# Kernel tuning notes

Hardware: AMD Instinct MI355X
Metric: run time of the kernel (lower is better)

## Reference

```python
import jax, jax.numpy as jnp
import numpy as np

EPS = 1.1920929e-07  # torch RMSNorm default eps = float32 finfo eps

def rms_norm(x, w):
    return x * jax.lax.rsqrt(jnp.mean(x * x, axis=-1, keepdims=True) + EPS) * w

def setup_inputs() -> dict:
    key = jax.random.key(0)
    ks = jax.random.split(key, 10)
    B, C, H, W = 8, 64, 48, 48
    E = C  # embed_dim = query_dim = key_dim = value_dim
    q = jax.random.normal(ks[0], (B, C, H, W), jnp.float32)
    k = jax.random.normal(ks[1], (B, C, H, W), jnp.float32)
    v = jax.random.normal(ks[2], (B, C, H, W), jnp.float32)
    s = 1.0 / np.sqrt(E)
    conv_w = jax.random.normal(ks[3], (C, C, 3, 3), jnp.float32) * (1.0 / np.sqrt(C * 9))
    nq_w = jnp.ones((E,), jnp.float32)
    nk_w = jnp.ones((E,), jnp.float32)
    wq = jax.random.normal(ks[4], (E, E), jnp.float32) * s
    bq = jax.random.normal(ks[5], (E,), jnp.float32) * 0.01
    wk = jax.random.normal(ks[6], (E, E), jnp.float32) * s
    bk = jax.random.normal(ks[7], (E,), jnp.float32) * 0.01
    return {"q": q, "k": k, "v": v, "conv_w": conv_w, "nq_w": nq_w,
            "nk_w": nk_w, "wq": wq, "bq": bq, "wk": wk, "bk": bk}

def reference(q, k, v, conv_w, nq_w, nk_w, wq, bq, wk, bk):
    B, C, H, W = q.shape
    num_heads = 4
    head_dim = C // num_heads
    # conv2d 3x3, stride 1, same padding, no bias
    qc = jax.lax.conv_general_dilated(
        q, conv_w, window_strides=(1, 1), padding='SAME',
        dimension_numbers=('NCHW', 'OIHW', 'NCHW'))
    # b c h w -> b (h w) c
    qs = qc.reshape(B, C, H * W).transpose(0, 2, 1)
    ksq = k.reshape(B, C, -1).transpose(0, 2, 1)
    vsq = v.reshape(B, C, -1).transpose(0, 2, 1)
    # RMSNorm on q and k (norm_v output feeds MHA value path whose output is discarded)
    qn = rms_norm(qs, nq_w)
    kn = rms_norm(ksq, nk_w)
    # MHA projections (q scaled by 1/sqrt(head_dim) as in torch)
    qp = (qn @ wq.T + bq) * (1.0 / np.sqrt(head_dim))
    kp = ksq_p = kn @ wk.T + bk
    Sq, Sk = qp.shape[1], kp.shape[1]
    qh = qp.reshape(B, Sq, num_heads, head_dim)
    kh = kp.reshape(B, Sk, num_heads, head_dim)
    scores = jnp.einsum('bihd,bjhd->bhij', qh, kh)
    attn = jax.nn.softmax(scores, axis=-1)
    # average_attn_weights=True -> mean over heads
    attn_avg = jnp.mean(attn, axis=1)  # [b, i, j]
    # custom output: weighted sum over RAW (un-normed, unprojected) value
    out = jnp.einsum('bij,bjd->bid', attn_avg, vsq)
    return out
```

## Files before the change

### kernel.cpp

```cpp
#include <hip/hip_runtime.h>
#include <hip/hip_bf16.h>

namespace {
constexpr int kB = 8;
constexpr int kC = 64;
constexpr int kH = 48;
constexpr int kW = 48;
constexpr int kS = kH * kW;
constexpr float kEps = 1.1920929e-07f;
constexpr float kQScale = 0.25f * 1.4426950408889634f;
}

typedef __attribute__((ext_vector_type(8))) short short8;
typedef __attribute__((ext_vector_type(4))) float f32x4;

__device__ __forceinline__ short f2bf(float x) {
  unsigned u = __float_as_uint(x);
  u += 0x7fffu + ((u >> 16) & 1u);
  return (short)(u >> 16);
}
__device__ __forceinline__ float bf2f(short s) {
  return __uint_as_float(((unsigned)(unsigned short)s) << 16);
}
__device__ __forceinline__ float fexp2(float x) {
  return __builtin_amdgcn_exp2f(x);
}

__global__ __launch_bounds__(256) void fused_prep(
    const float* __restrict__ q, const float* __restrict__ k,
    const float* __restrict__ v, const float* __restrict__ wq,
    const float* __restrict__ wk, const float* __restrict__ conv_w,
    short* __restrict__ qt, short* __restrict__ kt, short* __restrict__ vq,
    short* __restrict__ wqb3, short* __restrict__ wkb3, short* __restrict__ wt3) {
  const int blk = blockIdx.x;
  if (blk < 576) {
    __shared__ float tile[64][65];
    const int zz = blk / 36;
    const int bx = blk % 36;
    const int b = zz >> 1;
    const float* src = (zz & 1) ? k : q;
    short* dst = (zz & 1) ? kt : qt;
    const int s0 = bx * 64;
    const int tx = threadIdx.x & 63;
    const int ty = threadIdx.x >> 6;
#pragma unroll
    for (int r = 0; r < 16; ++r) {
      int c = r * 4 + ty;
      tile[c][tx] = src[((size_t)b * kC + c) * kS + s0 + tx];
    }
    __syncthreads();
#pragma unroll
    for (int r = 0; r < 16; ++r) {
      int s = r * 4 + ty;
      dst[((size_t)b * kS + s0 + s) * kC + tx] = f2bf(tile[tx][s]);
    }
  } else if (blk < 1152) {
    int g = (blk - 576) * 256 + threadIdx.x;
    int bb = g / 18432;
    int rem = g - bb * 18432;
    int jseg = rem >> 8;
    int sub = rem & 255;
    int d = sub >> 6;
    int Lq = sub & 63;
    const float* src = v + ((size_t)(bb * 64 + d * 16 + (Lq & 15))) * kS
                         + jseg * 32 + (Lq >> 4) * 8;
    float4 x0 = *reinterpret_cast<const float4*>(src);
    float4 x1 = *reinterpret_cast<const float4*>(src + 4);
    short8 o;
    o[0] = f2bf(x0.x); o[1] = f2bf(x0.y); o[2] = f2bf(x0.z); o[3] = f2bf(x0.w);
    o[4] = f2bf(x1.x); o[5] = f2bf(x1.y); o[6] = f2bf(x1.z); o[7] = f2bf(x1.w);
    *reinterpret_cast<short8*>(vq + (size_t)g * 8) = o;
  } else {
    int idx = (blk - 1152) * 256 + threadIdx.x;
    if (idx < 4096) {
      int j = idx & 7, Lw = (idx >> 3) & 63, slab = idx >> 9;
      int nt = slab & 3, kh = slab >> 2;
      int e = nt * 16 + (Lw & 15), c = kh * 32 + (Lw >> 4) * 8 + j;
      wqb3[idx] = f2bf(wq[e * 64 + c]);
    } else if (idx < 8192) {
      int i2 = idx - 4096;
      int j = i2 & 7, Lw = (i2 >> 3) & 63, slab = i2 >> 9;
      int nt = slab & 3, kh = slab >> 2;
      int e = nt * 16 + (Lw & 15), c = kh * 32 + (Lw >> 4) * 8 + j;
      wkb3[i2] = f2bf(wk[e * 64 + c]);
    } else {
      int i3 = idx - 8192;
      int j = i3 & 7, Lw = (i3 >> 3) & 63, slab = i3 >> 9;
      int nt = slab & 3, kh = (slab >> 2) & 1, tap = slab >> 3;
      int co = nt * 16 + (Lw & 15), ci = kh * 32 + (Lw >> 4) * 8 + j;
      wt3[i3] = f2bf(conv_w[co * 576 + ci * 9 + tap]);
    }
  }
}

__global__ __launch_bounds__(256) void fused_qk_gemm(
    const short* __restrict__ qt, const short* __restrict__ kt,
    const short* __restrict__ wt3, const short* __restrict__ wqb3,
    const short* __restrict__ wkb3,
    const float* __restrict__ nq_w, const float* __restrict__ nk_w,
    const float* __restrict__ bq, const float* __restrict__ bk,
    short* __restrict__ qp, short* __restrict__ kq) {
  __shared__ __align__(16) short Qs[164][72];
  __shared__ __align__(16) short ln[4][16][80];
  const int blk = blockIdx.x;
  const int t = threadIdx.x;
  const int ws = t >> 6;
  const int L = t & 63;
  const int quad = L >> 4;
  const int l16 = L & 15;
  const short8 zero8 = {0, 0, 0, 0, 0, 0, 0, 0};

  if (blk < 288) {
    const int b = blk / 36;
    const int S0 = (blk % 36) * 64;
    const int sBase = S0 + ws * 16;
    const int s = sBase + l16;
    const int h = s / kW, w = s % kW;

    const short* qtb = qt + (size_t)b * kS * kC;
#pragma unroll
    for (int it = 0; it < 6; ++it) {
      int idx = it * 256 + t;
      if (idx < 164 * 8) {
        int r = idx >> 3, sg = idx & 7;
        int srow = S0 - 49 + r;
        srow = srow < 0 ? 0 : (srow >= kS ? kS - 1 : srow);
        *reinterpret_cast<int4*>(&Qs[r][sg * 8]) =
            *reinterpret_cast<const int4*>(qtb + (size_t)srow * kC + sg * 8);
      }
    }
    __syncthreads();

    const int baseLocal = ws * 16 + l16 + 49;
    f32x4 acc[4] = {{0.f, 0.f, 0.f, 0.f}, {0.f, 0.f, 0.f, 0.f},
                    {0.f, 0.f, 0.f, 0.f}, {0.f, 0.f, 0.f, 0.f}};
#pragma unroll
    for (int tap = 0; tap < 9; ++tap) {
      const int dh = tap / 3 - 1, dw = tap % 3 - 1;
      const bool valid = (unsigned)(h + dh) < (unsigned)kH &&
                         (unsigned)(w + dw) < (unsigned)kW;
      const int local = baseLocal + dh * kW + dw;
#pragma unroll
      for (int kh = 0; kh < 2; ++kh) {
        short8 af = *reinterpret_cast<const short8*>(&Qs[local][kh * 32 + quad * 8]);
        af = valid ? af : zero8;
        const short* wb = wt3 + ((tap * 2 + kh) * 4) * 512 + L * 8;
#pragma unroll
        for (int nt = 0; nt < 4; ++nt) {
          short8 bf = *reinterpret_cast<const short8*>(wb + nt * 512);
          acc[nt] = __builtin_amdgcn_mfma_f32_16x16x32_bf16(af, bf, acc[nt], 0, 0, 0);
        }
      }
    }
    float rstd[4];
#pragma unroll
    for (int reg = 0; reg < 4; ++reg) {
      float pr = acc[0][reg] * acc[0][reg] + acc[1][reg] * acc[1][reg]
               + acc[2][reg] * acc[2][reg] + acc[3][reg] * acc[3][reg];
      pr += __shfl_xor(pr, 1, 64);
      pr += __shfl_xor(pr, 2, 64);
      pr += __shfl_xor(pr, 4, 64);
      pr += __shfl_xor(pr, 8, 64);
      rstd[reg] = rsqrtf(pr * (1.0f / kC) + kEps);
    }
#pragma unroll
    for (int nt = 0; nt < 4; ++nt) {
      float g = nq_w[nt * 16 + l16];
#pragma unroll
      for (int reg = 0; reg < 4; ++reg) {
        ln[ws][quad * 4 + reg][nt * 16 + l16] = f2bf(acc[nt][reg] * rstd[reg] * g);
      }
    }
    __syncthreads();
    f32x4 acc2[4] = {{0.f, 0.f, 0.f, 0.f}, {0.f, 0.f, 0.f, 0.f},
                     {0.f, 0.f, 0.f, 0.f}, {0.f, 0.f, 0.f, 0.f}};
#pragma unroll
    for (int kh = 0; kh < 2; ++kh) {
      short8 af = *reinterpret_cast<const short8*>(&ln[ws][l16][kh * 32 + quad * 8]);
      const short* wb = wqb3 + (kh * 4) * 512 + L * 8;
#pragma unroll
      for (int nt = 0; nt < 4; ++nt) {
        short8 bf = *reinterpret_cast<const short8*>(wb + nt * 512);
        acc2[nt] = __builtin_amdgcn_mfma_f32_16x16x32_bf16(af, bf, acc2[nt], 0, 0, 0);
      }
    }
#pragma unroll
    for (int nt = 0; nt < 4; ++nt) {
      const int e = nt * 16 + l16;
      float bias = bq[e];
#pragma unroll
      for (int reg = 0; reg < 4; ++reg) {
        qp[((size_t)b * kS + sBase + quad * 4 + reg) * kC + e] =
            f2bf((acc2[nt][reg] + bias) * kQScale);
      }
    }
  } else {
    const int idx = blk - 288;
    const int b = idx / 36;
    const int S0 = (idx % 36) * 64;
    const int sBase = S0 + ws * 16;

    const short* ktb = kt + ((size_t)b * kS + S0) * kC;
#pragma unroll
    for (int it = 0; it < 2; ++it) {
      int r = it * 32 + (t >> 3), sg = t & 7;
      *reinterpret_cast<int4*>(&Qs[r][sg * 8]) =
          *reinterpret_cast<const int4*>(ktb + (size_t)r * kC + sg * 8);
    }
    __syncthreads();

    short8 af0 = *reinterpret_cast<const short8*>(&Qs[ws * 16 + l16][quad * 8]);
    short8 af1 = *reinterpret_cast<const short8*>(&Qs[ws * 16 + l16][32 + quad * 8]);

    float xs[16];
#pragma unroll
    for (int j = 0; j < 8; ++j) { xs[j] = bf2f(af0[j]); xs[8 + j] = bf2f(af1[j]); }
    float sum = 0.f;
#pragma unroll
    for (int j = 0; j < 16; ++j) sum = fmaf(xs[j], xs[j], sum);
    sum += __shfl_xor(sum, 16, 64);
    sum += __shfl_xor(sum, 32, 64);
    float rstd = rsqrtf(sum * (1.0f / kC) + kEps);

    const float* n0 = nk_w + quad * 8;
#pragma unroll
    for (int j = 0; j < 8; ++j) {
      af0[j] = f2bf(xs[j] * rstd * n0[j]);
      af1[j] = f2bf(xs[8 + j] * rstd * n0[32 + j]);
    }

    f32x4 acc[4] = {{0.f, 0.f, 0.f, 0.f}, {0.f, 0.f, 0.f, 0.f},
                    {0.f, 0.f, 0.f, 0.f}, {0.f, 0.f, 0.f, 0.f}};
#pragma unroll
    for (int nt = 0; nt < 4; ++nt) {
      short8 bf0 = *reinterpret_cast<const short8*>(
          wkb3 + (0 * 4 + nt) * 512 + L * 8);
      short8 bf1 = *reinterpret_cast<const short8*>(
          wkb3 + (1 * 4 + nt) * 512 + L * 8);
      acc[nt] = __builtin_amdgcn_mfma_f32_16x16x32_bf16(af0, bf0, acc[nt], 0, 0, 0);
      acc[nt] = __builtin_amdgcn_mfma_f32_16x16x32_bf16(af1, bf1, acc[nt], 0, 0, 0);
    }
    short* kqb = kq + (size_t)b * 147456;
#pragma unroll
    for (int nt = 0; nt < 4; ++nt) {
      const int e = nt * 16 + l16;
      const int hp = nt >> 1;
      const int quadp = ((nt & 1) << 1) | (l16 >> 3);
      const int elem = l16 & 7;
      float bias = bk[e];
#pragma unroll
      for (int reg = 0; reg < 4; ++reg) {
        int s = sBase + quad * 4 + reg;
        int jseg = s >> 5, jrow = s & 31;
        int c = (jrow >> 2) & 1;
        int l16p = ((jrow >> 3) << 2) | (jrow & 3);
        kqb[((((size_t)jseg * 2 + hp) * 2 + c) * 64 + quadp * 16 + l16p) * 8 + elem] =
            f2bf(acc[nt][reg] + bias);
      }
    }
  }
}

__global__ __launch_bounds__(256, 4) void attn_flash(
    const short* __restrict__ qp, const short* __restrict__ kq,
    const short* __restrict__ vq, float* __restrict__ out) {
  __shared__ float pl[4][16][2];
  __shared__ float Li[32][2];
  __shared__ __align__(16) float slab[16][66];

  const int blk = blockIdx.x;
  const int b = blk & 7;
  const int idx = blk >> 3;
  const int hp = idx & 1;
  const int i0 = (idx >> 1) * 32;
  const int t = threadIdx.x;
  const int ws = t >> 6;
  const int isub = ws & 1;
  const int jhalf = ws >> 1;
  const int L = t & 63;
  const int quad = L >> 4;
  const int l16 = L & 15;

  const f32x4 zc = {0.f, 0.f, 0.f, 0.f};
  const short8 z8 = {0, 0, 0, 0, 0, 0, 0, 0};

  const short* qrow = qp + ((size_t)b * kS + i0 + isub * 16 + l16) * kC + hp * 32;
  const short8 qw = *reinterpret_cast<const short8*>(qrow + quad * 8);
  const bool lo = quad < 2;
  const short8 qm[2] = {lo ? qw : z8, lo ? z8 : qw};

  const short* kbase =
      kq + (((size_t)(b * 72 + jhalf) * 2 + hp) * 2 * 64 + L) * 8;
  const short* vbase = vq + ((size_t)(b * 72 + jhalf) * 4 * 64 + L) * 8;

  f32x4 U[2][4];
#pragma unroll
  for (int hl = 0; hl < 2; ++hl)
#pragma unroll
    for (int d = 0; d < 4; ++d) U[hl][d] = zc;
  float lh[2] = {0.f, 0.f};

  short8 kn[2], vn[4];
#pragma unroll
  for (int c = 0; c < 2; ++c)
    kn[c] = *reinterpret_cast<const short8*>(kbase + c * 512);
#pragma unroll
  for (int d = 0; d < 4; ++d)
    vn[d] = *reinterpret_cast<const short8*>(vbase + d * 512);

  for (int jt = 0; jt < kS / 64; ++jt) {
    const short8 kf0 = kn[0], kf1 = kn[1];
    const short8 vf0 = vn[0], vf1 = vn[1], vf2 = vn[2], vf3 = vn[3];

    if (jt + 1 < kS / 64) {
      const short* kb2 = kbase + (size_t)(jt + 1) * 4096;
      const short* vb2 = vbase + (size_t)(jt + 1) * 4096;
#pragma unroll
      for (int c = 0; c < 2; ++c)
        kn[c] = *reinterpret_cast<const short8*>(kb2 + c * 512);
#pragma unroll
      for (int d = 0; d < 4; ++d)
        vn[d] = *reinterpret_cast<const short8*>(vb2 + d * 512);
    }

#pragma unroll
    for (int hl = 0; hl < 2; ++hl) {
      f32x4 s0 = __builtin_amdgcn_mfma_f32_16x16x32_bf16(kf0, qm[hl], zc, 0, 0, 0);
      f32x4 s1 = __builtin_amdgcn_mfma_f32_16x16x32_bf16(kf1, qm[hl], zc, 0, 0, 0);
      float e0 = fexp2(s0[0]), e1 = fexp2(s0[1]);
      float e2 = fexp2(s0[2]), e3 = fexp2(s0[3]);
      float f0 = fexp2(s1[0]), f1 = fexp2(s1[1]);
      float f2 = fexp2(s1[2]), f3 = fexp2(s1[3]);
      lh[hl] += ((e0 + e1) + (e2 + e3)) + ((f0 + f1) + (f2 + f3));
      union { __hip_bfloat162 h2[4]; short8 s8; } cv;
      cv.h2[0] = __float22bfloat162_rn(make_float2(e0, e1));
      cv.h2[1] = __float22bfloat162_rn(make_float2(e2, e3));
      cv.h2[2] = __float22bfloat162_rn(make_float2(f0, f1));
      cv.h2[3] = __float22bfloat162_rn(make_float2(f2, f3));
      U[hl][0] = __builtin_amdgcn_mfma_f32_16x16x32_bf16(vf0, cv.s8, U[hl][0], 0, 0, 0);
      U[hl][1] = __builtin_amdgcn_mfma_f32_16x16x32_bf16(vf1, cv.s8, U[hl][1], 0, 0, 0);
      U[hl][2] = __builtin_amdgcn_mfma_f32_16x16x32_bf16(vf2, cv.s8, U[hl][2], 0, 0, 0);
      U[hl][3] = __builtin_amdgcn_mfma_f32_16x16x32_bf16(vf3, cv.s8, U[hl][3], 0, 0, 0);
    }
  }

#pragma unroll
  for (int hl = 0; hl < 2; ++hl) {
    lh[hl] += __shfl_xor(lh[hl], 16, 64);
    lh[hl] += __shfl_xor(lh[hl], 32, 64);
  }
  if (quad == 0) {
#pragma unroll
    for (int hl = 0; hl < 2; ++hl) pl[ws][l16][hl] = lh[hl];
  }
  __syncthreads();
  if (t < 64) {
    const int i = t >> 1, h2 = t & 1;
    Li[i][h2] = 0.25f / (pl[i >> 4][i & 15][h2] + pl[(i >> 4) + 2][i & 15][h2]);
  }
  __syncthreads();
  float c2[2];
#pragma unroll
  for (int hl = 0; hl < 2; ++hl) c2[hl] = Li[isub * 16 + l16][hl];

#pragma unroll
  for (int d = 0; d < 4; ++d) {
    if (jhalf == 1) {
#pragma unroll
      for (int hl = 0; hl < 2; ++hl)
#pragma unroll
        for (int reg = 0; reg < 4; ++reg)
          slab[(isub * 2 + hl) * 4 + reg][L] = U[hl][d][reg];
    }
    __syncthreads();
    if (jhalf == 0) {
      float of[4] = {0.f, 0.f, 0.f, 0.f};
#pragma unroll
      for (int hl = 0; hl < 2; ++hl) {
#pragma unroll
        for (int reg = 0; reg < 4; ++reg) {
          float tot = U[hl][d][reg] + slab[(isub * 2 + hl) * 4 + reg][L];
          of[reg] += tot * c2[hl];
        }
      }
      float* op = out + ((size_t)b * kS + i0 + isub * 16 + l16) * kC + d * 16 + quad * 4;
#pragma unroll
      for (int reg = 0; reg < 4; ++reg) atomicAdd(op + reg, of[reg]);
    }
    __syncthreads();
  }
}

extern "C" void kernel_launch(void* const* d_in, const int* in_sizes, int n_in,
                              void* d_out, int out_size, void* d_ws, size_t ws_size,
                              hipStream_t stream) {
  const float* q      = (const float*)d_in[0];
  const float* k      = (const float*)d_in[1];
  const float* v      = (const float*)d_in[2];
  const float* conv_w = (const float*)d_in[3];
  const float* nq_w   = (const float*)d_in[4];
  const float* nk_w   = (const float*)d_in[5];
  const float* wq     = (const float*)d_in[6];
  const float* bq     = (const float*)d_in[7];
  const float* wk     = (const float*)d_in[8];
  const float* bk     = (const float*)d_in[9];
  float* out = (float*)d_out;

  const size_t N = (size_t)kB * kS * kC;
  short* qt   = (short*)d_ws;
  short* kt   = qt + N;
  short* vq   = kt + N;
  short* qp   = vq + N;
  short* kq   = qp + N;
  short* wqb3 = kq + N;
  short* wkb3 = wqb3 + 4096;
  short* wt3  = wkb3 + 4096;

  hipMemsetAsync(d_out, 0, out_size, stream);

  fused_prep<<<1328, 256, 0, stream>>>(q, k, v, wq, wk, conv_w,
                                       qt, kt, vq, wqb3, wkb3, wt3);
  fused_qk_gemm<<<576, 256, 0, stream>>>(qt, kt, wt3, wqb3, wkb3,
                                         nq_w, nk_w, bq, bk, qp, kq);
  attn_flash<<<1152, 256, 0, stream>>>(qp, kq, vq, out);
}
```

Measured before the change: 152.2 us.

## Double-buffer K/V loads and compute softmax row sums via extra MFMA

Replaces the single-stage prefetch loop with a two-slot register double buffer, unrolled in pairs of tiles, so loads for tile j+2 are issued while tile j+1 is computed. The per-lane VALU row-sum of the exponentials and its cross-lane shuffle reduction are replaced by an extra MFMA against a ones vector masked to lane 0, which accumulates the denominator on the matrix unit. The denominator now sums bf16-rounded probabilities instead of fp32 ones, and the extra MFMA per phase adds matrix work plus register pressure that may affect occupancy at the 4-waves launch bound.

```diff
diff --git a/kernel.cpp b/kernel.cpp
--- a/kernel.cpp
+++ b/kernel.cpp
@@ -261,6 +261,41 @@
   }
 }
 
+#define LOADT(K0, K1, V0, V1, V2, V3, JT)                                      \
+  do {                                                                         \
+    const short* kb_ = kbase + (size_t)(JT) * 4096;                            \
+    const short* vb_ = vbase + (size_t)(JT) * 4096;                            \
+    K0 = *reinterpret_cast<const short8*>(kb_);                                \
+    K1 = *reinterpret_cast<const short8*>(kb_ + 512);                          \
+    V0 = *reinterpret_cast<const short8*>(vb_);                                \
+    V1 = *reinterpret_cast<const short8*>(vb_ + 512);                          \
+    V2 = *reinterpret_cast<const short8*>(vb_ + 1024);                         \
+    V3 = *reinterpret_cast<const short8*>(vb_ + 1536);                         \
+  } while (0)
+
+#define PHASE(K0, K1, V0, V1, V2, V3)                                          \
+  do {                                                                         \
+    _Pragma("unroll")                                                          \
+    for (int hl = 0; hl < 2; ++hl) {                                           \
+      f32x4 s0 = __builtin_amdgcn_mfma_f32_16x16x32_bf16(K0, qm[hl], zc, 0, 0, 0); \
+      f32x4 s1 = __builtin_amdgcn_mfma_f32_16x16x32_bf16(K1, qm[hl], zc, 0, 0, 0); \
+      float e0 = fexp2(s0[0]), e1 = fexp2(s0[1]);                              \
+      float e2 = fexp2(s0[2]), e3 = fexp2(s0[3]);                              \
+      float f0 = fexp2(s1[0]), f1 = fexp2(s1[1]);                              \
+      float f2 = fexp2(s1[2]), f3 = fexp2(s1[3]);                              \
+      union { __hip_bfloat162 h2[4]; short8 s8; } cv;                          \
+      cv.h2[0] = __float22bfloat162_rn(make_float2(e0, e1));                   \
+      cv.h2[1] = __float22bfloat162_rn(make_float2(e2, e3));                   \
+      cv.h2[2] = __float22bfloat162_rn(make_float2(f0, f1));                   \
+      cv.h2[3] = __float22bfloat162_rn(make_float2(f2, f3));                   \
+      U[hl][0] = __builtin_amdgcn_mfma_f32_16x16x32_bf16(V0, cv.s8, U[hl][0], 0, 0, 0); \
+      U[hl][1] = __builtin_amdgcn_mfma_f32_16x16x32_bf16(V1, cv.s8, U[hl][1], 0, 0, 0); \
+      U[hl][2] = __builtin_amdgcn_mfma_f32_16x16x32_bf16(V2, cv.s8, U[hl][2], 0, 0, 0); \
+      U[hl][3] = __builtin_amdgcn_mfma_f32_16x16x32_bf16(V3, cv.s8, U[hl][3], 0, 0, 0); \
+      Ul[hl]   = __builtin_amdgcn_mfma_f32_16x16x32_bf16(af_l, cv.s8, Ul[hl], 0, 0, 0); \
+    }                                                                          \
+  } while (0)
+
 __global__ __launch_bounds__(256, 4) void attn_flash(
     const short* __restrict__ qp, const short* __restrict__ kq,
     const short* __restrict__ vq, float* __restrict__ out) {
@@ -283,6 +318,9 @@
 
   const f32x4 zc = {0.f, 0.f, 0.f, 0.f};
   const short8 z8 = {0, 0, 0, 0, 0, 0, 0, 0};
+  const short ob = (short)0x3F80;
+  const short8 ones8 = {ob, ob, ob, ob, ob, ob, ob, ob};
+  const short8 af_l = (l16 == 0) ? ones8 : z8;
 
   const short* qrow = qp + ((size_t)b * kS + i0 + isub * 16 + l16) * kC + hp * 32;
   const short8 qw = *reinterpret_cast<const short8*>(qrow + quad * 8);
@@ -298,60 +336,25 @@
   for (int hl = 0; hl < 2; ++hl)
 #pragma unroll
     for (int d = 0; d < 4; ++d) U[hl][d] = zc;
-  float lh[2] = {0.f, 0.f};
-
-  short8 kn[2], vn[4];
-#pragma unroll
-  for (int c = 0; c < 2; ++c)
-    kn[c] = *reinterpret_cast<const short8*>(kbase + c * 512);
-#pragma unroll
-  for (int d = 0; d < 4; ++d)
-    vn[d] = *reinterpret_cast<const short8*>(vbase + d * 512);
-
-  for (int jt = 0; jt < kS / 64; ++jt) {
-    const short8 kf0 = kn[0], kf1 = kn[1];
-    const short8 vf0 = vn[0], vf1 = vn[1], vf2 = vn[2], vf3 = vn[3];
-
-    if (jt + 1 < kS / 64) {
-      const short* kb2 = kbase + (size_t)(jt + 1) * 4096;
-      const short* vb2 = vbase + (size_t)(jt + 1) * 4096;
-#pragma unroll
-      for (int c = 0; c < 2; ++c)
-        kn[c] = *reinterpret_cast<const short8*>(kb2 + c * 512);
-#pragma unroll
-      for (int d = 0; d < 4; ++d)
-        vn[d] = *reinterpret_cast<const short8*>(vb2 + d * 512);
-    }
-
-#pragma unroll
-    for (int hl = 0; hl < 2; ++hl) {
-      f32x4 s0 = __builtin_amdgcn_mfma_f32_16x16x32_bf16(kf0, qm[hl], zc, 0, 0, 0);
-      f32x4 s1 = __builtin_amdgcn_mfma_f32_16x16x32_bf16(kf1, qm[hl], zc, 0, 0, 0);
-      float e0 = fexp2(s0[0]), e1 = fexp2(s0[1]);
-      float e2 = fexp2(s0[2]), e3 = fexp2(s0[3]);
-      float f0 = fexp2(s1[0]), f1 = fexp2(s1[1]);
-      float f2 = fexp2(s1[2]), f3 = fexp2(s1[3]);
-      lh[hl] += ((e0 + e1) + (e2 + e3)) + ((f0 + f1) + (f2 + f3));
-      union { __hip_bfloat162 h2[4]; short8 s8; } cv;
-      cv.h2[0] = __float22bfloat162_rn(make_float2(e0, e1));
-      cv.h2[1] = __float22bfloat162_rn(make_float2(e2, e3));
-      cv.h2[2] = __float22bfloat162_rn(make_float2(f0, f1));
-      cv.h2[3] = __float22bfloat162_rn(make_float2(f2, f3));
-      U[hl][0] = __builtin_amdgcn_mfma_f32_16x16x32_bf16(vf0, cv.s8, U[hl][0], 0, 0, 0);
-      U[hl][1] = __builtin_amdgcn_mfma_f32_16x16x32_bf16(vf1, cv.s8, U[hl][1], 0, 0, 0);
-      U[hl][2] = __builtin_amdgcn_mfma_f32_16x16x32_bf16(vf2, cv.s8, U[hl][2], 0, 0, 0);
-      U[hl][3] = __builtin_amdgcn_mfma_f32_16x16x32_bf16(vf3, cv.s8, U[hl][3], 0, 0, 0);
-    }
-  }
-
-#pragma unroll
-  for (int hl = 0; hl < 2; ++hl) {
-    lh[hl] += __shfl_xor(lh[hl], 16, 64);
-    lh[hl] += __shfl_xor(lh[hl], 32, 64);
-  }
+  f32x4 Ul[2] = {zc, zc};
+
+  short8 ka0, ka1, va0, va1, va2, va3;
+  short8 kb0, kb1, vb0, vb1, vb2, vb3;
+  LOADT(ka0, ka1, va0, va1, va2, va3, 0);
+  LOADT(kb0, kb1, vb0, vb1, vb2, vb3, 1);
+
+  for (int jt = 0; jt < 34; jt += 2) {
+    PHASE(ka0, ka1, va0, va1, va2, va3);
+    LOADT(ka0, ka1, va0, va1, va2, va3, jt + 2);
+    PHASE(kb0, kb1, vb0, vb1, vb2, vb3);
+    LOADT(kb0, kb1, vb0, vb1, vb2, vb3, jt + 3);
+  }
+  PHASE(ka0, ka1, va0, va1, va2, va3);
+  PHASE(kb0, kb1, vb0, vb1, vb2, vb3);
+
   if (quad == 0) {
 #pragma unroll
-    for (int hl = 0; hl < 2; ++hl) pl[ws][l16][hl] = lh[hl];
+    for (int hl = 0; hl < 2; ++hl) pl[ws][l16][hl] = Ul[hl][0];
   }
   __syncthreads();
   if (t < 64) {
```

Measured after the change: 148.6 us. 2.4% less time.
